# Performance work log

Hardware: AMD Instinct MI355X
Metric: run time of the kernel (lower is better)

The kernel has to match this reference:

```python
import jax, jax.numpy as jnp
import numpy as np

N, E = 10000, 320000
IN, H, C, ED = 256, 4, 64, 64
HC = H * C
EPS = 1e-5
NEG_SLOPE = 0.2


def setup_inputs() -> dict:
    key = jax.random.key(0)
    ks = jax.random.split(key, 12)
    g = lambda k, shape, fan: jax.random.normal(k, shape, jnp.float32) * (1.0 / np.sqrt(fan))
    return {
        "x": jax.random.normal(ks[0], (N, IN), jnp.float32),
        "edge_index": jax.random.randint(ks[1], (2, E), 0, N, jnp.int64),
        "edge_attr": jax.random.normal(ks[2], (E, ED), jnp.float32),
        "Wl": g(ks[3], (HC, IN), IN),   # lin_l weight (source)
        "bl": jnp.zeros((HC,), jnp.float32),
        "Wr": g(ks[4], (HC, IN), IN),   # lin_r weight (target)
        "br": jnp.zeros((HC,), jnp.float32),
        "We": g(ks[5], (HC, ED), ED),   # lin_edge weight (no bias)
        "att": g(ks[6], (H, C), C),
        "bias": jnp.zeros((HC,), jnp.float32),
        "gamma": jnp.ones((HC,), jnp.float32),
        "beta": jnp.zeros((HC,), jnp.float32),
    }


def reference(x, edge_index, edge_attr, Wl, bl, Wr, br, We, att, bias, gamma, beta):
    src, dst = edge_index[0], edge_index[1]
    # add_self_loops with fill_value='mean': loop edge_attr = mean of incoming attrs
    ones = jnp.ones((E,), jnp.float32)
    cnt = jax.ops.segment_sum(ones, dst, num_segments=N)              # [N]
    loop_attr = jax.ops.segment_sum(edge_attr, dst, num_segments=N) / jnp.maximum(cnt, 1.0)[:, None]
    node_ids = jnp.arange(N, dtype=src.dtype)
    src_f = jnp.concatenate([src, node_ids])                          # [E+N]
    dst_f = jnp.concatenate([dst, node_ids])
    ea = jnp.concatenate([edge_attr, loop_attr], axis=0)              # [E+N, ED]

    xl = (x @ Wl.T + bl).reshape(N, H, C)   # source-side projection
    xr = (x @ Wr.T + br).reshape(N, H, C)   # target-side projection
    ep = (ea @ We.T).reshape(-1, H, C)       # edge projection

    m = xl[src_f] + xr[dst_f] + ep                                    # [E+N, H, C]
    m = jnp.where(m >= 0, m, NEG_SLOPE * m)                           # leaky_relu(0.2)
    logits = jnp.einsum("ehc,hc->eh", m, att)                        # [E+N, H]

    # segment softmax over target node dst_f (every node has a self loop)
    mx = jax.ops.segment_max(logits, dst_f, num_segments=N)
    ex = jnp.exp(logits - mx[dst_f])
    den = jax.ops.segment_sum(ex, dst_f, num_segments=N)
    alpha = ex / den[dst_f]                                           # [E+N, H]

    out = jax.ops.segment_sum(xl[src_f] * alpha[:, :, None], dst_f, num_segments=N)
    h = out.reshape(N, HC) + bias

    # SiLU then LayerNorm, dropout is identity in eval
    h = h * jax.nn.sigmoid(h)
    mu = jnp.mean(h, axis=-1, keepdims=True)
    var = jnp.mean((h - mu) ** 2, axis=-1, keepdims=True)
    h = (h - mu) * jax.lax.rsqrt(var + EPS) * gamma + beta
    return h, alpha
```

## Files before the change

### kernel.cpp

```cpp
#include <hip/hip_runtime.h>

#define N_NODES 10000
#define N_EDGES 320000
#define NE_TOT  330000
#define NEG_SLOPE 0.2f
#define LN_EPS 1e-5f

#define OFF_CNT    0u
#define OFF_FILL   40000u
#define OFF_ROWPTR 80128u
#define OFF_EIDS   120320u
#define OFF_POSE   1440512u
#define OFF_XLH    4000512u
#define OFF_XRH    9120512u
#define OFF_LOG    14240512u
#define OFF_WLF    19520512u
#define OFF_WRF    19651584u
#define OFF_WEF    19782656u
#define OFF_SD     19815424u
#define OFF_EAC    21135424u

typedef __bf16 bf16x8 __attribute__((ext_vector_type(8)));
typedef float  f32x4  __attribute__((ext_vector_type(4)));
typedef unsigned short us4 __attribute__((ext_vector_type(4)));

__device__ __forceinline__ float bf2f(unsigned short u) {
    union { unsigned int i; float f; } v;
    v.i = ((unsigned int)u) << 16;
    return v.f;
}
__device__ __forceinline__ unsigned short f2bf(float x) {
    __bf16 b = (__bf16)x;
    return __builtin_bit_cast(unsigned short, b);
}
__device__ __forceinline__ bf16x8 cvt8(const float* p) {
    float4 v0 = *reinterpret_cast<const float4*>(p);
    float4 v1 = *reinterpret_cast<const float4*>(p + 4);
    bf16x8 t;
    t[0] = (__bf16)v0.x; t[1] = (__bf16)v0.y; t[2] = (__bf16)v0.z; t[3] = (__bf16)v0.w;
    t[4] = (__bf16)v1.x; t[5] = (__bf16)v1.y; t[6] = (__bf16)v1.z; t[7] = (__bf16)v1.w;
    return t;
}

__global__ void k_count(const int* __restrict__ ei, int* __restrict__ cnt) {
    int e = blockIdx.x * blockDim.x + threadIdx.x;
    if (e < N_EDGES) atomicAdd(&cnt[ei[N_EDGES + e]], 1);
}

__global__ void k_scan(const int* __restrict__ cnt, int* __restrict__ row_ptr) {
    __shared__ int sums[1024];
    int t = threadIdx.x;
    const int CH = 10;
    int base = t * CH;
    int s = 0;
    for (int i = 0; i < CH; i++) {
        int n = base + i;
        if (n < N_NODES) s += cnt[n] + 1;
    }
    sums[t] = s;
    __syncthreads();
    for (int off = 1; off < 1024; off <<= 1) {
        int v = (t >= off) ? sums[t - off] : 0;
        __syncthreads();
        sums[t] += v;
        __syncthreads();
    }
    int run = (t == 0) ? 0 : sums[t - 1];
    for (int i = 0; i < CH; i++) {
        int n = base + i;
        if (n < N_NODES) { row_ptr[n] = run; run += cnt[n] + 1; }
    }
    if (t == 1023) row_ptr[N_NODES] = sums[1023];
}

__global__ void k_fill(const int* __restrict__ ei, const int* __restrict__ row_ptr,
                       int* __restrict__ fill, int* __restrict__ eids,
                       int* __restrict__ sdv, int* __restrict__ pose) {
    int e = blockIdx.x * blockDim.x + threadIdx.x;
    if (e >= NE_TOT) return;
    int s, d;
    if (e < N_EDGES) { s = ei[e]; d = ei[N_EDGES + e]; }
    else             { s = e - N_EDGES; d = s; }
    int pos = atomicAdd(&fill[d], 1);
    int p = row_ptr[d] + pos;
    eids[p] = e;
    sdv[p] = s | (d << 16);
    pose[e] = p;
}

__global__ void k_permute_e(const float* __restrict__ edge_attr,
                            const int* __restrict__ pose,
                            unsigned short* __restrict__ eac) {
    int idx = blockIdx.x * blockDim.x + threadIdx.x;
    if (idx >= N_EDGES * 32) return;
    int e = idx >> 5, cp = idx & 31;
    float2 v = reinterpret_cast<const float2*>(edge_attr)[(size_t)e * 32 + cp];
    int p = pose[e];
    unsigned int u = ((unsigned int)f2bf(v.x)) | (((unsigned int)f2bf(v.y)) << 16);
    reinterpret_cast<unsigned int*>(eac)[(size_t)p * 32 + cp] = u;
}

__global__ void k_self_attr(const int* __restrict__ row_ptr,
                            const int* __restrict__ pose,
                            unsigned short* __restrict__ eac) {
    int node = (blockIdx.x << 2) + (threadIdx.x >> 6);
    int lane = threadIdx.x & 63;
    int b = row_ptr[node], en = row_ptr[node + 1];
    int selfp = pose[N_EDGES + node];
    float s0 = 0.0f, s1 = 0.0f;
    int i = b;
    for (; i + 1 < en; i += 2) {
        float a0 = bf2f(eac[(size_t)(i + 0) * 64 + lane]);
        float a1 = bf2f(eac[(size_t)(i + 1) * 64 + lane]);
        s0 += (i + 0 == selfp) ? 0.0f : a0;
        s1 += (i + 1 == selfp) ? 0.0f : a1;
    }
    for (; i < en; i++) {
        float a = bf2f(eac[(size_t)i * 64 + lane]);
        s0 += (i == selfp) ? 0.0f : a;
    }
    float s = s0 + s1;
    float c = (float)(en - b - 1);
    eac[(size_t)selfp * 64 + lane] = f2bf(s / fmaxf(c, 1.0f));
}

__global__ void k_prep_wfrag(const float* __restrict__ Wl,
                             const float* __restrict__ Wr,
                             const float* __restrict__ We,
                             unsigned short* __restrict__ wlf,
                             unsigned short* __restrict__ wrf,
                             unsigned short* __restrict__ wef) {
    int idx = blockIdx.x * 256 + threadIdx.x;
    if (idx >= 8192) return;
    int ln = idx & 63;
    int ts = (idx >> 6) & 7;
    int ct = idx >> 9;
    int c = ct * 16 + (ln & 15);
    int k0 = ts * 32 + (ln >> 4) * 8;
    *reinterpret_cast<bf16x8*>(wlf + (size_t)idx * 8) = cvt8(Wl + (size_t)c * 256 + k0);
    *reinterpret_cast<bf16x8*>(wrf + (size_t)idx * 8) = cvt8(Wr + (size_t)c * 256 + k0);
    if (idx < 2048) {
        int f = idx >> 6;
        int cb = f >> 1, step = f & 1;
        int ce = cb * 16 + (ln & 15);
        int ke = step * 32 + (ln >> 4) * 8;
        *reinterpret_cast<bf16x8*>(wef + (size_t)idx * 8) = cvt8(We + (size_t)ce * 64 + ke);
    }
}

__global__ __launch_bounds__(256) void k_gemm_mfma(
        const float* __restrict__ x,
        const float* __restrict__ bl, const float* __restrict__ br,
        const unsigned short* __restrict__ wlf,
        const unsigned short* __restrict__ wrf,
        unsigned short* __restrict__ xlh,
        unsigned short* __restrict__ xrh) {
    __shared__ __bf16 xs[8 * 64 * 8];
    int tid = threadIdx.x;
    int nb = blockIdx.x * 16;

    for (int f = tid; f < 512; f += 256) {
        int t = f >> 6, ln = f & 63;
        int node = nb + (ln & 15);
        int k0 = t * 32 + (ln >> 4) * 8;
        *reinterpret_cast<bf16x8*>(&xs[f * 8]) = cvt8(x + (size_t)node * 256 + k0);
    }
    __syncthreads();

    int lane = tid & 63;
    int wv = tid >> 6;
    int quad = lane >> 4;
    int ln15 = lane & 15;

    bf16x8 bfr[8];
#pragma unroll
    for (int t = 0; t < 8; t++)
        bfr[t] = *reinterpret_cast<const bf16x8*>(&xs[(t * 64 + lane) * 8]);

    int node = nb + ln15;
#pragma unroll
    for (int ci = 0; ci < 4; ci++) {
        int ct = wv * 4 + ci;
        f32x4 accl, accr;
        accl[0] = accl[1] = accl[2] = accl[3] = 0.0f;
        accr[0] = accr[1] = accr[2] = accr[3] = 0.0f;
#pragma unroll
        for (int t = 0; t < 8; t++) {
            bf16x8 al = *reinterpret_cast<const bf16x8*>(
                wlf + ((size_t)(ct * 8 + t) * 64 + lane) * 8);
            accl = __builtin_amdgcn_mfma_f32_16x16x32_bf16(al, bfr[t], accl, 0, 0, 0);
        }
#pragma unroll
        for (int t = 0; t < 8; t++) {
            bf16x8 ar = *reinterpret_cast<const bf16x8*>(
                wrf + ((size_t)(ct * 8 + t) * 64 + lane) * 8);
            accr = __builtin_amdgcn_mfma_f32_16x16x32_bf16(ar, bfr[t], accr, 0, 0, 0);
        }
        int cbase = ct * 16 + quad * 4;
        float4 blv = *reinterpret_cast<const float4*>(bl + cbase);
        float4 brv = *reinterpret_cast<const float4*>(br + cbase);
        us4 ol, orr;
        ol[0] = f2bf(accl[0] + blv.x); ol[1] = f2bf(accl[1] + blv.y);
        ol[2] = f2bf(accl[2] + blv.z); ol[3] = f2bf(accl[3] + blv.w);
        orr[0] = f2bf(accr[0] + brv.x); orr[1] = f2bf(accr[1] + brv.y);
        orr[2] = f2bf(accr[2] + brv.z); orr[3] = f2bf(accr[3] + brv.w);
        *reinterpret_cast<us4*>(xlh + (size_t)node * 256 + cbase) = ol;
        *reinterpret_cast<us4*>(xrh + (size_t)node * 256 + cbase) = orr;
    }
}

__global__ __launch_bounds__(256) void k_logits_mfma(
        const int* __restrict__ sdv,
        const unsigned short* __restrict__ eac,
        const unsigned short* __restrict__ xlh,
        const unsigned short* __restrict__ xrh,
        const unsigned short* __restrict__ wef,
        const float* __restrict__ att,
        float* __restrict__ logits) {
    __shared__ __bf16 wef_s[2048 * 8];
    __shared__ float att_s[256];
    int tid = threadIdx.x;

    for (int f = tid; f < 2048; f += 256) {
        *reinterpret_cast<bf16x8*>(&wef_s[(size_t)f * 8]) =
            *reinterpret_cast<const bf16x8*>(wef + (size_t)f * 8);
    }
    if (tid < 64) {
        reinterpret_cast<float4*>(att_s)[tid] =
            reinterpret_cast<const float4*>(att)[tid];
    }
    __syncthreads();

    int lane = tid & 63;
    int wv = tid >> 6;
    int quad = lane >> 4;
    int ln15 = lane & 15;

    const int ntiles = NE_TOT / 16;
#pragma unroll 1
    for (int t = blockIdx.x * 4 + wv; t < ntiles; t += gridDim.x * 4) {
        int pos = t * 16 + ln15;
        int sd = sdv[pos];
        int s = sd & 0xFFFF;
        int d = sd >> 16;
        const unsigned short* row = eac + (size_t)pos * 64;
        const unsigned short* xls = xlh + (size_t)s * 256;
        const unsigned short* xrd = xrh + (size_t)d * 256;

        bf16x8 bfr0 = *reinterpret_cast<const bf16x8*>(row + quad * 8);
        bf16x8 bfr1 = *reinterpret_cast<const bf16x8*>(row + 32 + quad * 8);
        us4 xa[16], xb[16];
#pragma unroll
        for (int cb = 0; cb < 16; cb++) {
            int cbase = cb * 16 + quad * 4;
            xa[cb] = *reinterpret_cast<const us4*>(xls + cbase);
            xb[cb] = *reinterpret_cast<const us4*>(xrd + cbase);
        }
        __builtin_amdgcn_sched_barrier(0);

        float hsum[4] = {0.0f, 0.0f, 0.0f, 0.0f};
#pragma unroll
        for (int cb = 0; cb < 16; cb++) {
            f32x4 acc;
            acc[0] = acc[1] = acc[2] = acc[3] = 0.0f;
            bf16x8 a0 = *reinterpret_cast<const bf16x8*>(
                &wef_s[((size_t)(cb * 2 + 0) * 64 + lane) * 8]);
            bf16x8 a1 = *reinterpret_cast<const bf16x8*>(
                &wef_s[((size_t)(cb * 2 + 1) * 64 + lane) * 8]);
            acc = __builtin_amdgcn_mfma_f32_16x16x32_bf16(a0, bfr0, acc, 0, 0, 0);
            acc = __builtin_amdgcn_mfma_f32_16x16x32_bf16(a1, bfr1, acc, 0, 0, 0);

            int cbase = cb * 16 + quad * 4;
            float4 at = *reinterpret_cast<const float4*>(&att_s[cbase]);
            const float* tp = reinterpret_cast<const float*>(&at);
            float hs = 0.0f;
#pragma unroll
            for (int r = 0; r < 4; r++) {
                float v = acc[r] + bf2f(xa[cb][r]) + bf2f(xb[cb][r]);
                v = fmaxf(v, NEG_SLOPE * v);
                hs = fmaf(v, tp[r], hs);
            }
            hsum[cb >> 2] += hs;
        }
#pragma unroll
        for (int hh = 0; hh < 4; hh++) {
            hsum[hh] += __shfl_xor(hsum[hh], 16, 64);
            hsum[hh] += __shfl_xor(hsum[hh], 32, 64);
        }
        if (quad == 0) {
            reinterpret_cast<float4*>(logits)[pos] =
                make_float4(hsum[0], hsum[1], hsum[2], hsum[3]);
        }
    }
}

__global__ void k_aggregate(const int* __restrict__ sdv,
                            const int* __restrict__ row_ptr,
                            const int* __restrict__ eids,
                            const float* __restrict__ logits,
                            const unsigned short* __restrict__ xlh,
                            const float* __restrict__ bias,
                            const float* __restrict__ gamma,
                            const float* __restrict__ beta,
                            float* __restrict__ hout,
                            float* __restrict__ alpha_out) {
    int node = (blockIdx.x << 2) + (threadIdx.x >> 6);
    int lane = threadIdx.x & 63;
    int h = lane >> 4;
    int b = row_ptr[node], en = row_ptr[node + 1];

    float m0 = -INFINITY, m1 = -INFINITY, m2 = -INFINITY, m3 = -INFINITY;
    int i = b;
    for (; i + 3 < en; i += 4) {
        m0 = fmaxf(m0, logits[(i + 0) * 4 + h]);
        m1 = fmaxf(m1, logits[(i + 1) * 4 + h]);
        m2 = fmaxf(m2, logits[(i + 2) * 4 + h]);
        m3 = fmaxf(m3, logits[(i + 3) * 4 + h]);
    }
    for (; i < en; i++) m0 = fmaxf(m0, logits[i * 4 + h]);
    float mh = fmaxf(fmaxf(m0, m1), fmaxf(m2, m3));

    float d0 = 0.0f, d1 = 0.0f, d2 = 0.0f, d3 = 0.0f;
    i = b;
    for (; i + 3 < en; i += 4) {
        d0 += __expf(logits[(i + 0) * 4 + h] - mh);
        d1 += __expf(logits[(i + 1) * 4 + h] - mh);
        d2 += __expf(logits[(i + 2) * 4 + h] - mh);
        d3 += __expf(logits[(i + 3) * 4 + h] - mh);
    }
    for (; i < en; i++) d0 += __expf(logits[i * 4 + h] - mh);
    float rden = 1.0f / ((d0 + d1) + (d2 + d3));

    int c0 = lane * 4;
    float4 ac0; ac0.x = ac0.y = ac0.z = ac0.w = 0.0f;
    float4 ac1; ac1.x = ac1.y = ac1.z = ac1.w = 0.0f;
    float4 ac2; ac2.x = ac2.y = ac2.z = ac2.w = 0.0f;
    float4 ac3; ac3.x = ac3.y = ac3.z = ac3.w = 0.0f;
    i = b;
    for (; i + 3 < en; i += 4) {
        int e0 = eids[i], e1 = eids[i + 1], e2 = eids[i + 2], e3 = eids[i + 3];
        float al0 = __expf(logits[(i + 0) * 4 + h] - mh) * rden;
        float al1 = __expf(logits[(i + 1) * 4 + h] - mh) * rden;
        float al2 = __expf(logits[(i + 2) * 4 + h] - mh) * rden;
        float al3 = __expf(logits[(i + 3) * 4 + h] - mh) * rden;
        if ((lane & 15) == 0) {
            alpha_out[e0 * 4 + h] = al0;
            alpha_out[e1 * 4 + h] = al1;
            alpha_out[e2 * 4 + h] = al2;
            alpha_out[e3 * 4 + h] = al3;
        }
        int s0 = sdv[i + 0] & 0xFFFF;
        int s1 = sdv[i + 1] & 0xFFFF;
        int s2 = sdv[i + 2] & 0xFFFF;
        int s3 = sdv[i + 3] & 0xFFFF;
        us4 x0 = *reinterpret_cast<const us4*>(xlh + (size_t)s0 * 256 + c0);
        us4 x1 = *reinterpret_cast<const us4*>(xlh + (size_t)s1 * 256 + c0);
        us4 x2 = *reinterpret_cast<const us4*>(xlh + (size_t)s2 * 256 + c0);
        us4 x3 = *reinterpret_cast<const us4*>(xlh + (size_t)s3 * 256 + c0);
        ac0.x = fmaf(al0, bf2f(x0[0]), ac0.x); ac0.y = fmaf(al0, bf2f(x0[1]), ac0.y);
        ac0.z = fmaf(al0, bf2f(x0[2]), ac0.z); ac0.w = fmaf(al0, bf2f(x0[3]), ac0.w);
        ac1.x = fmaf(al1, bf2f(x1[0]), ac1.x); ac1.y = fmaf(al1, bf2f(x1[1]), ac1.y);
        ac1.z = fmaf(al1, bf2f(x1[2]), ac1.z); ac1.w = fmaf(al1, bf2f(x1[3]), ac1.w);
        ac2.x = fmaf(al2, bf2f(x2[0]), ac2.x); ac2.y = fmaf(al2, bf2f(x2[1]), ac2.y);
        ac2.z = fmaf(al2, bf2f(x2[2]), ac2.z); ac2.w = fmaf(al2, bf2f(x2[3]), ac2.w);
        ac3.x = fmaf(al3, bf2f(x3[0]), ac3.x); ac3.y = fmaf(al3, bf2f(x3[1]), ac3.y);
        ac3.z = fmaf(al3, bf2f(x3[2]), ac3.z); ac3.w = fmaf(al3, bf2f(x3[3]), ac3.w);
    }
    for (; i < en; i++) {
        int e = eids[i];
        float al = __expf(logits[i * 4 + h] - mh) * rden;
        if ((lane & 15) == 0) alpha_out[e * 4 + h] = al;
        int s = sdv[i] & 0xFFFF;
        us4 xv = *reinterpret_cast<const us4*>(xlh + (size_t)s * 256 + c0);
        ac0.x = fmaf(al, bf2f(xv[0]), ac0.x); ac0.y = fmaf(al, bf2f(xv[1]), ac0.y);
        ac0.z = fmaf(al, bf2f(xv[2]), ac0.z); ac0.w = fmaf(al, bf2f(xv[3]), ac0.w);
    }
    float4 acc;
    acc.x = (ac0.x + ac1.x) + (ac2.x + ac3.x);
    acc.y = (ac0.y + ac1.y) + (ac2.y + ac3.y);
    acc.z = (ac0.z + ac1.z) + (ac2.z + ac3.z);
    acc.w = (ac0.w + ac1.w) + (ac2.w + ac3.w);

    const float4 b4 = reinterpret_cast<const float4*>(bias)[lane];
    float4 hv;
    hv.x = acc.x + b4.x; hv.y = acc.y + b4.y;
    hv.z = acc.z + b4.z; hv.w = acc.w + b4.w;
    hv.x = hv.x / (1.0f + __expf(-hv.x));
    hv.y = hv.y / (1.0f + __expf(-hv.y));
    hv.z = hv.z / (1.0f + __expf(-hv.z));
    hv.w = hv.w / (1.0f + __expf(-hv.w));
    float s1 = hv.x + hv.y + hv.z + hv.w;
    float s2 = hv.x * hv.x + hv.y * hv.y + hv.z * hv.z + hv.w * hv.w;
#pragma unroll
    for (int off = 1; off < 64; off <<= 1) {
        s1 += __shfl_xor(s1, off, 64);
        s2 += __shfl_xor(s2, off, 64);
    }
    float mu = s1 * (1.0f / 256.0f);
    float var = s2 * (1.0f / 256.0f) - mu * mu;
    float rs = rsqrtf(var + LN_EPS);
    const float4 g4 = reinterpret_cast<const float4*>(gamma)[lane];
    const float4 be4 = reinterpret_cast<const float4*>(beta)[lane];
    float4 o;
    o.x = (hv.x - mu) * rs * g4.x + be4.x;
    o.y = (hv.y - mu) * rs * g4.y + be4.y;
    o.z = (hv.z - mu) * rs * g4.z + be4.z;
    o.w = (hv.w - mu) * rs * g4.w + be4.w;
    reinterpret_cast<float4*>(hout)[node * 64 + lane] = o;
}

extern "C" void kernel_launch(void* const* d_in, const int* in_sizes, int n_in,
                              void* d_out, int out_size, void* d_ws, size_t ws_size,
                              hipStream_t stream) {
    (void)in_sizes; (void)n_in; (void)out_size; (void)ws_size;
    const float* x         = (const float*)d_in[0];
    const int*   ei        = (const int*)d_in[1];
    const float* edge_attr = (const float*)d_in[2];
    const float* Wl        = (const float*)d_in[3];
    const float* bl        = (const float*)d_in[4];
    const float* Wr        = (const float*)d_in[5];
    const float* br        = (const float*)d_in[6];
    const float* We        = (const float*)d_in[7];
    const float* att       = (const float*)d_in[8];
    const float* bias      = (const float*)d_in[9];
    const float* gamma     = (const float*)d_in[10];
    const float* beta      = (const float*)d_in[11];

    char* ws = (char*)d_ws;
    int*   cnt     = (int*)(ws + OFF_CNT);
    int*   fill    = (int*)(ws + OFF_FILL);
    int*   row_ptr = (int*)(ws + OFF_ROWPTR);
    int*   eids    = (int*)(ws + OFF_EIDS);
    int*   pose    = (int*)(ws + OFF_POSE);
    unsigned short* xlh = (unsigned short*)(ws + OFF_XLH);
    unsigned short* xrh = (unsigned short*)(ws + OFF_XRH);
    float* logits  = (float*)(ws + OFF_LOG);
    unsigned short* wlf = (unsigned short*)(ws + OFF_WLF);
    unsigned short* wrf = (unsigned short*)(ws + OFF_WRF);
    unsigned short* wef = (unsigned short*)(ws + OFF_WEF);
    int*   sdv     = (int*)(ws + OFF_SD);
    unsigned short* eac = (unsigned short*)(ws + OFF_EAC);

    float* hout      = (float*)d_out;
    float* alpha_out = (float*)d_out + N_NODES * 256;

    hipMemsetAsync(ws + OFF_CNT, 0, 2 * N_NODES * sizeof(int), stream);

    k_count<<<(N_EDGES + 255) / 256, 256, 0, stream>>>(ei, cnt);
    k_scan<<<1, 1024, 0, stream>>>(cnt, row_ptr);
    k_prep_wfrag<<<32, 256, 0, stream>>>(Wl, Wr, We, wlf, wrf, wef);
    k_fill<<<(NE_TOT + 255) / 256, 256, 0, stream>>>(ei, row_ptr, fill, eids, sdv, pose);
    k_gemm_mfma<<<N_NODES / 16, 256, 0, stream>>>(x, bl, br, wlf, wrf, xlh, xrh);
    k_permute_e<<<(N_EDGES * 32) / 256, 256, 0, stream>>>(edge_attr, pose, eac);
    k_self_attr<<<N_NODES / 4, 256, 0, stream>>>(row_ptr, pose, eac);
    k_logits_mfma<<<2048, 256, 0, stream>>>(sdv, eac, xlh, xrh, wef, att, logits);
    k_aggregate<<<N_NODES / 4, 256, 0, stream>>>(sdv, row_ptr, eids, logits, xlh,
                                                 bias, gamma, beta, hout, alpha_out);
}
```

Before: 354.0 us.

## Split edge projection GEMM out and fuse logits with per-node softmax aggregation

The edge-attribute projection is now a standalone MFMA GEMM that writes a bf16 projected-edge buffer (E+N by 256). Logit computation moves into the per-node aggregation kernel: each wave computes its node's incoming edge logits, keeps them in shared memory (or a global buffer for degree above 256), then does softmax and the weighted sum in the same kernel. This removes the separate logits pass and the global logits round-trip, and xr is loaded once per destination node. In exchange, a roughly 170MB bf16 edge-projection intermediate is written and read back, which may cost more memory traffic than it saves.

```diff
diff --git a/kernel.cpp b/kernel.cpp
--- a/kernel.cpp
+++ b/kernel.cpp
@@ -19,6 +19,7 @@
 #define OFF_WEF    19782656u
 #define OFF_SD     19815424u
 #define OFF_EAC    21135424u
+#define OFF_EPC    63375424u
 
 typedef __bf16 bf16x8 __attribute__((ext_vector_type(8)));
 typedef float  f32x4  __attribute__((ext_vector_type(4)));
@@ -27,6 +28,16 @@
 __device__ __forceinline__ float bf2f(unsigned short u) {
     union { unsigned int i; float f; } v;
     v.i = ((unsigned int)u) << 16;
+    return v.f;
+}
+__device__ __forceinline__ float lo2f(unsigned int u) {
+    union { unsigned int i; float f; } v;
+    v.i = u << 16;
+    return v.f;
+}
+__device__ __forceinline__ float hi2f(unsigned int u) {
+    union { unsigned int i; float f; } v;
+    v.i = u & 0xFFFF0000u;
     return v.f;
 }
 __device__ __forceinline__ unsigned short f2bf(float x) {
@@ -209,25 +220,15 @@
     }
 }
 
-__global__ __launch_bounds__(256) void k_logits_mfma(
-        const int* __restrict__ sdv,
+__global__ __launch_bounds__(256) void k_ep_gemm(
         const unsigned short* __restrict__ eac,
-        const unsigned short* __restrict__ xlh,
-        const unsigned short* __restrict__ xrh,
         const unsigned short* __restrict__ wef,
-        const float* __restrict__ att,
-        float* __restrict__ logits) {
+        unsigned short* __restrict__ epc) {
     __shared__ __bf16 wef_s[2048 * 8];
-    __shared__ float att_s[256];
     int tid = threadIdx.x;
-
     for (int f = tid; f < 2048; f += 256) {
         *reinterpret_cast<bf16x8*>(&wef_s[(size_t)f * 8]) =
             *reinterpret_cast<const bf16x8*>(wef + (size_t)f * 8);
-    }
-    if (tid < 64) {
-        reinterpret_cast<float4*>(att_s)[tid] =
-            reinterpret_cast<const float4*>(att)[tid];
     }
     __syncthreads();
 
@@ -240,25 +241,10 @@
 #pragma unroll 1
     for (int t = blockIdx.x * 4 + wv; t < ntiles; t += gridDim.x * 4) {
         int pos = t * 16 + ln15;
-        int sd = sdv[pos];
-        int s = sd & 0xFFFF;
-        int d = sd >> 16;
         const unsigned short* row = eac + (size_t)pos * 64;
-        const unsigned short* xls = xlh + (size_t)s * 256;
-        const unsigned short* xrd = xrh + (size_t)d * 256;
-
-        bf16x8 bfr0 = *reinterpret_cast<const bf16x8*>(row + quad * 8);
-        bf16x8 bfr1 = *reinterpret_cast<const bf16x8*>(row + 32 + quad * 8);
-        us4 xa[16], xb[16];
-#pragma unroll
-        for (int cb = 0; cb < 16; cb++) {
-            int cbase = cb * 16 + quad * 4;
-            xa[cb] = *reinterpret_cast<const us4*>(xls + cbase);
-            xb[cb] = *reinterpret_cast<const us4*>(xrd + cbase);
-        }
-        __builtin_amdgcn_sched_barrier(0);
-
-        float hsum[4] = {0.0f, 0.0f, 0.0f, 0.0f};
+        bf16x8 b0 = *reinterpret_cast<const bf16x8*>(row + quad * 8);
+        bf16x8 b1 = *reinterpret_cast<const bf16x8*>(row + 32 + quad * 8);
+        unsigned short* orow = epc + (size_t)pos * 256;
 #pragma unroll
         for (int cb = 0; cb < 16; cb++) {
             f32x4 acc;
@@ -267,124 +253,150 @@
                 &wef_s[((size_t)(cb * 2 + 0) * 64 + lane) * 8]);
             bf16x8 a1 = *reinterpret_cast<const bf16x8*>(
                 &wef_s[((size_t)(cb * 2 + 1) * 64 + lane) * 8]);
-            acc = __builtin_amdgcn_mfma_f32_16x16x32_bf16(a0, bfr0, acc, 0, 0, 0);
-            acc = __builtin_amdgcn_mfma_f32_16x16x32_bf16(a1, bfr1, acc, 0, 0, 0);
-
-            int cbase = cb * 16 + quad * 4;
-            float4 at = *reinterpret_cast<const float4*>(&att_s[cbase]);
-            const float* tp = reinterpret_cast<const float*>(&at);
-            float hs = 0.0f;
-#pragma unroll
-            for (int r = 0; r < 4; r++) {
-                float v = acc[r] + bf2f(xa[cb][r]) + bf2f(xb[cb][r]);
-                v = fmaxf(v, NEG_SLOPE * v);
-                hs = fmaf(v, tp[r], hs);
+            acc = __builtin_amdgcn_mfma_f32_16x16x32_bf16(a0, b0, acc, 0, 0, 0);
+            acc = __builtin_amdgcn_mfma_f32_16x16x32_bf16(a1, b1, acc, 0, 0, 0);
+            us4 o;
+            o[0] = f2bf(acc[0]); o[1] = f2bf(acc[1]);
+            o[2] = f2bf(acc[2]); o[3] = f2bf(acc[3]);
+            *reinterpret_cast<us4*>(orow + cb * 16 + quad * 4) = o;
+        }
+    }
+}
+
+__device__ __forceinline__ float edge_logit(uint2 xlv, uint2 epv,
+        float xra, float xrb, float xrc, float xrd, float4 atv) {
+    float v0 = lo2f(xlv.x) + xra + lo2f(epv.x); v0 = fmaxf(v0, NEG_SLOPE * v0);
+    float v1 = hi2f(xlv.x) + xrb + hi2f(epv.x); v1 = fmaxf(v1, NEG_SLOPE * v1);
+    float v2 = lo2f(xlv.y) + xrc + lo2f(epv.y); v2 = fmaxf(v2, NEG_SLOPE * v2);
+    float v3 = hi2f(xlv.y) + xrd + hi2f(epv.y); v3 = fmaxf(v3, NEG_SLOPE * v3);
+    float hs = fmaf(v0, atv.x, fmaf(v1, atv.y, fmaf(v2, atv.z, v3 * atv.w)));
+    hs += __shfl_xor(hs, 1, 64);
+    hs += __shfl_xor(hs, 2, 64);
+    hs += __shfl_xor(hs, 4, 64);
+    hs += __shfl_xor(hs, 8, 64);
+    return hs;
+}
+
+__global__ __launch_bounds__(256) void k_node_fused(
+        const int* __restrict__ sdv,
+        const int* __restrict__ row_ptr,
+        const int* __restrict__ eids,
+        const unsigned short* __restrict__ epc,
+        const unsigned short* __restrict__ xlh,
+        const unsigned short* __restrict__ xrh,
+        const float* __restrict__ att,
+        const float* __restrict__ bias,
+        const float* __restrict__ gamma,
+        const float* __restrict__ beta,
+        float* __restrict__ lbuf,
+        float* __restrict__ hout,
+        float* __restrict__ alpha_out) {
+    __shared__ float lsc[4][1024];
+    int tid = threadIdx.x;
+    int wv = tid >> 6, lane = tid & 63;
+    int node = blockIdx.x * 4 + wv;
+    int h = lane >> 4, l15 = lane & 15;
+    int b = row_ptr[node], en = row_ptr[node + 1];
+    int len = en - b;
+    bool big = len > 256;
+    float* ls = lsc[wv];
+
+    const uint2* xl2 = reinterpret_cast<const uint2*>(xlh);
+    const uint2* ep2 = reinterpret_cast<const uint2*>(epc);
+    float4 atv = reinterpret_cast<const float4*>(att)[lane];
+    uint2 xrv = reinterpret_cast<const uint2*>(xrh)[(size_t)node * 64 + lane];
+    float xra = lo2f(xrv.x), xrb = hi2f(xrv.x);
+    float xrc = lo2f(xrv.y), xrd = hi2f(xrv.y);
+
+    int i = b;
+    for (; i + 1 < en; i += 2) {
+        int sd0 = sdv[i], sd1 = sdv[i + 1];
+        int s0 = sd0 & 0xFFFF, s1 = sd1 & 0xFFFF;
+        uint2 xl0 = xl2[(size_t)s0 * 64 + lane];
+        uint2 e0v = ep2[(size_t)i * 64 + lane];
+        uint2 xl1 = xl2[(size_t)s1 * 64 + lane];
+        uint2 e1v = ep2[(size_t)(i + 1) * 64 + lane];
+        float h0 = edge_logit(xl0, e0v, xra, xrb, xrc, xrd, atv);
+        float h1 = edge_logit(xl1, e1v, xra, xrb, xrc, xrd, atv);
+        if (l15 == 0) {
+            if (!big) {
+                ls[(i - b) * 4 + h] = h0;
+                ls[(i + 1 - b) * 4 + h] = h1;
+            } else {
+                lbuf[(size_t)i * 4 + h] = h0;
+                lbuf[(size_t)(i + 1) * 4 + h] = h1;
             }
-            hsum[cb >> 2] += hs;
-        }
-#pragma unroll
-        for (int hh = 0; hh < 4; hh++) {
-            hsum[hh] += __shfl_xor(hsum[hh], 16, 64);
-            hsum[hh] += __shfl_xor(hsum[hh], 32, 64);
-        }
-        if (quad == 0) {
-            reinterpret_cast<float4*>(logits)[pos] =
-                make_float4(hsum[0], hsum[1], hsum[2], hsum[3]);
-        }
-    }
-}
-
-__global__ void k_aggregate(const int* __restrict__ sdv,
-                            const int* __restrict__ row_ptr,
-                            const int* __restrict__ eids,
-                            const float* __restrict__ logits,
-                            const unsigned short* __restrict__ xlh,
-                            const float* __restrict__ bias,
-                            const float* __restrict__ gamma,
-                            const float* __restrict__ beta,
-                            float* __restrict__ hout,
-                            float* __restrict__ alpha_out) {
-    int node = (blockIdx.x << 2) + (threadIdx.x >> 6);
-    int lane = threadIdx.x & 63;
-    int h = lane >> 4;
-    int b = row_ptr[node], en = row_ptr[node + 1];
-
-    float m0 = -INFINITY, m1 = -INFINITY, m2 = -INFINITY, m3 = -INFINITY;
-    int i = b;
-    for (; i + 3 < en; i += 4) {
-        m0 = fmaxf(m0, logits[(i + 0) * 4 + h]);
-        m1 = fmaxf(m1, logits[(i + 1) * 4 + h]);
-        m2 = fmaxf(m2, logits[(i + 2) * 4 + h]);
-        m3 = fmaxf(m3, logits[(i + 3) * 4 + h]);
-    }
-    for (; i < en; i++) m0 = fmaxf(m0, logits[i * 4 + h]);
-    float mh = fmaxf(fmaxf(m0, m1), fmaxf(m2, m3));
-
-    float d0 = 0.0f, d1 = 0.0f, d2 = 0.0f, d3 = 0.0f;
+        }
+    }
+    if (i < en) {
+        int sd0 = sdv[i];
+        int s0 = sd0 & 0xFFFF;
+        uint2 xl0 = xl2[(size_t)s0 * 64 + lane];
+        uint2 e0v = ep2[(size_t)i * 64 + lane];
+        float h0 = edge_logit(xl0, e0v, xra, xrb, xrc, xrd, atv);
+        if (l15 == 0) {
+            if (!big) ls[(i - b) * 4 + h] = h0;
+            else      lbuf[(size_t)i * 4 + h] = h0;
+        }
+    }
+
+    float mh = -INFINITY;
+    for (int j = l15; j < len; j += 16) {
+        float lg = big ? lbuf[(size_t)(b + j) * 4 + h] : ls[j * 4 + h];
+        mh = fmaxf(mh, lg);
+    }
+    mh = fmaxf(mh, __shfl_xor(mh, 1, 64));
+    mh = fmaxf(mh, __shfl_xor(mh, 2, 64));
+    mh = fmaxf(mh, __shfl_xor(mh, 4, 64));
+    mh = fmaxf(mh, __shfl_xor(mh, 8, 64));
+    float den = 0.0f;
+    for (int j = l15; j < len; j += 16) {
+        float lg = big ? lbuf[(size_t)(b + j) * 4 + h] : ls[j * 4 + h];
+        den += __expf(lg - mh);
+    }
+    den += __shfl_xor(den, 1, 64);
+    den += __shfl_xor(den, 2, 64);
+    den += __shfl_xor(den, 4, 64);
+    den += __shfl_xor(den, 8, 64);
+    float rden = 1.0f / den;
+
+    float acx = 0.0f, acy = 0.0f, acz = 0.0f, acw = 0.0f;
     i = b;
-    for (; i + 3 < en; i += 4) {
-        d0 += __expf(logits[(i + 0) * 4 + h] - mh);
-        d1 += __expf(logits[(i + 1) * 4 + h] - mh);
-        d2 += __expf(logits[(i + 2) * 4 + h] - mh);
-        d3 += __expf(logits[(i + 3) * 4 + h] - mh);
-    }
-    for (; i < en; i++) d0 += __expf(logits[i * 4 + h] - mh);
-    float rden = 1.0f / ((d0 + d1) + (d2 + d3));
-
-    int c0 = lane * 4;
-    float4 ac0; ac0.x = ac0.y = ac0.z = ac0.w = 0.0f;
-    float4 ac1; ac1.x = ac1.y = ac1.z = ac1.w = 0.0f;
-    float4 ac2; ac2.x = ac2.y = ac2.z = ac2.w = 0.0f;
-    float4 ac3; ac3.x = ac3.y = ac3.z = ac3.w = 0.0f;
-    i = b;
-    for (; i + 3 < en; i += 4) {
-        int e0 = eids[i], e1 = eids[i + 1], e2 = eids[i + 2], e3 = eids[i + 3];
-        float al0 = __expf(logits[(i + 0) * 4 + h] - mh) * rden;
-        float al1 = __expf(logits[(i + 1) * 4 + h] - mh) * rden;
-        float al2 = __expf(logits[(i + 2) * 4 + h] - mh) * rden;
-        float al3 = __expf(logits[(i + 3) * 4 + h] - mh) * rden;
-        if ((lane & 15) == 0) {
-            alpha_out[e0 * 4 + h] = al0;
-            alpha_out[e1 * 4 + h] = al1;
-            alpha_out[e2 * 4 + h] = al2;
-            alpha_out[e3 * 4 + h] = al3;
-        }
-        int s0 = sdv[i + 0] & 0xFFFF;
-        int s1 = sdv[i + 1] & 0xFFFF;
-        int s2 = sdv[i + 2] & 0xFFFF;
-        int s3 = sdv[i + 3] & 0xFFFF;
-        us4 x0 = *reinterpret_cast<const us4*>(xlh + (size_t)s0 * 256 + c0);
-        us4 x1 = *reinterpret_cast<const us4*>(xlh + (size_t)s1 * 256 + c0);
-        us4 x2 = *reinterpret_cast<const us4*>(xlh + (size_t)s2 * 256 + c0);
-        us4 x3 = *reinterpret_cast<const us4*>(xlh + (size_t)s3 * 256 + c0);
-        ac0.x = fmaf(al0, bf2f(x0[0]), ac0.x); ac0.y = fmaf(al0, bf2f(x0[1]), ac0.y);
-        ac0.z = fmaf(al0, bf2f(x0[2]), ac0.z); ac0.w = fmaf(al0, bf2f(x0[3]), ac0.w);
-        ac1.x = fmaf(al1, bf2f(x1[0]), ac1.x); ac1.y = fmaf(al1, bf2f(x1[1]), ac1.y);
-        ac1.z = fmaf(al1, bf2f(x1[2]), ac1.z); ac1.w = fmaf(al1, bf2f(x1[3]), ac1.w);
-        ac2.x = fmaf(al2, bf2f(x2[0]), ac2.x); ac2.y = fmaf(al2, bf2f(x2[1]), ac2.y);
-        ac2.z = fmaf(al2, bf2f(x2[2]), ac2.z); ac2.w = fmaf(al2, bf2f(x2[3]), ac2.w);
-        ac3.x = fmaf(al3, bf2f(x3[0]), ac3.x); ac3.y = fmaf(al3, bf2f(x3[1]), ac3.y);
-        ac3.z = fmaf(al3, bf2f(x3[2]), ac3.z); ac3.w = fmaf(al3, bf2f(x3[3]), ac3.w);
-    }
-    for (; i < en; i++) {
-        int e = eids[i];
-        float al = __expf(logits[i * 4 + h] - mh) * rden;
-        if ((lane & 15) == 0) alpha_out[e * 4 + h] = al;
-        int s = sdv[i] & 0xFFFF;
-        us4 xv = *reinterpret_cast<const us4*>(xlh + (size_t)s * 256 + c0);
-        ac0.x = fmaf(al, bf2f(xv[0]), ac0.x); ac0.y = fmaf(al, bf2f(xv[1]), ac0.y);
-        ac0.z = fmaf(al, bf2f(xv[2]), ac0.z); ac0.w = fmaf(al, bf2f(xv[3]), ac0.w);
-    }
-    float4 acc;
-    acc.x = (ac0.x + ac1.x) + (ac2.x + ac3.x);
-    acc.y = (ac0.y + ac1.y) + (ac2.y + ac3.y);
-    acc.z = (ac0.z + ac1.z) + (ac2.z + ac3.z);
-    acc.w = (ac0.w + ac1.w) + (ac2.w + ac3.w);
+    for (; i + 1 < en; i += 2) {
+        int sd0 = sdv[i], sd1 = sdv[i + 1];
+        int e0 = eids[i], e1 = eids[i + 1];
+        int s0 = sd0 & 0xFFFF, s1 = sd1 & 0xFFFF;
+        uint2 xl0 = xl2[(size_t)s0 * 64 + lane];
+        uint2 xl1 = xl2[(size_t)s1 * 64 + lane];
+        float lg0 = big ? lbuf[(size_t)i * 4 + h]       : ls[(i - b) * 4 + h];
+        float lg1 = big ? lbuf[(size_t)(i + 1) * 4 + h] : ls[(i + 1 - b) * 4 + h];
+        float a0 = __expf(lg0 - mh) * rden;
+        float a1 = __expf(lg1 - mh) * rden;
+        if (l15 == 0) {
+            alpha_out[(size_t)e0 * 4 + h] = a0;
+            alpha_out[(size_t)e1 * 4 + h] = a1;
+        }
+        acx = fmaf(a0, lo2f(xl0.x), acx); acy = fmaf(a0, hi2f(xl0.x), acy);
+        acz = fmaf(a0, lo2f(xl0.y), acz); acw = fmaf(a0, hi2f(xl0.y), acw);
+        acx = fmaf(a1, lo2f(xl1.x), acx); acy = fmaf(a1, hi2f(xl1.x), acy);
+        acz = fmaf(a1, lo2f(xl1.y), acz); acw = fmaf(a1, hi2f(xl1.y), acw);
+    }
+    if (i < en) {
+        int sd0 = sdv[i];
+        int e0 = eids[i];
+        int s0 = sd0 & 0xFFFF;
+        uint2 xl0 = xl2[(size_t)s0 * 64 + lane];
+        float lg0 = big ? lbuf[(size_t)i * 4 + h] : ls[(i - b) * 4 + h];
+        float a0 = __expf(lg0 - mh) * rden;
+        if (l15 == 0) alpha_out[(size_t)e0 * 4 + h] = a0;
+        acx = fmaf(a0, lo2f(xl0.x), acx); acy = fmaf(a0, hi2f(xl0.x), acy);
+        acz = fmaf(a0, lo2f(xl0.y), acz); acw = fmaf(a0, hi2f(xl0.y), acw);
+    }
 
     const float4 b4 = reinterpret_cast<const float4*>(bias)[lane];
     float4 hv;
-    hv.x = acc.x + b4.x; hv.y = acc.y + b4.y;
-    hv.z = acc.z + b4.z; hv.w = acc.w + b4.w;
+    hv.x = acx + b4.x; hv.y = acy + b4.y;
+    hv.z = acz + b4.z; hv.w = acw + b4.w;
     hv.x = hv.x / (1.0f + __expf(-hv.x));
     hv.y = hv.y / (1.0f + __expf(-hv.y));
     hv.z = hv.z / (1.0f + __expf(-hv.z));
@@ -434,12 +446,13 @@
     int*   pose    = (int*)(ws + OFF_POSE);
     unsigned short* xlh = (unsigned short*)(ws + OFF_XLH);
     unsigned short* xrh = (unsigned short*)(ws + OFF_XRH);
-    float* logits  = (float*)(ws + OFF_LOG);
+    float* lbuf    = (float*)(ws + OFF_LOG);
     unsigned short* wlf = (unsigned short*)(ws + OFF_WLF);
     unsigned short* wrf = (unsigned short*)(ws + OFF_WRF);
     unsigned short* wef = (unsigned short*)(ws + OFF_WEF);
     int*   sdv     = (int*)(ws + OFF_SD);
     unsigned short* eac = (unsigned short*)(ws + OFF_EAC);
+    unsigned short* epc = (unsigned short*)(ws + OFF_EPC);
 
     float* hout      = (float*)d_out;
     float* alpha_out = (float*)d_out + N_NODES * 256;
@@ -453,7 +466,8 @@
     k_gemm_mfma<<<N_NODES / 16, 256, 0, stream>>>(x, bl, br, wlf, wrf, xlh, xrh);
     k_permute_e<<<(N_EDGES * 32) / 256, 256, 0, stream>>>(edge_attr, pose, eac);
     k_self_attr<<<N_NODES / 4, 256, 0, stream>>>(row_ptr, pose, eac);
-    k_logits_mfma<<<2048, 256, 0, stream>>>(sdv, eac, xlh, xrh, wef, att, logits);
-    k_aggregate<<<N_NODES / 4, 256, 0, stream>>>(sdv, row_ptr, eids, logits, xlh,
-                                                 bias, gamma, beta, hout, alpha_out);
-}
+    k_ep_gemm<<<1024, 256, 0, stream>>>(eac, wef, epc);
+    k_node_fused<<<N_NODES / 4, 256, 0, stream>>>(sdv, row_ptr, eids, epc, xlh, xrh,
+                                                  att, bias, gamma, beta, lbuf,
+                                                  hout, alpha_out);
+}
```

Result: slower. 380.6 us (+7.5%).
